# Performance work log

Measured on AMD Instinct MI355X. Metric: run time of the kernel, lower is better.

The kernel has to match this reference:

```python
import jax, jax.numpy as jnp
import numpy as np
from jax import lax

LATENT = 100
B, D, H, W = 32768, 120, 4, 2
BN_EPS = 1e-5


def setup_inputs() -> dict:
    key = jax.random.key(0)
    ks = jax.random.split(key, 12)
    inp = {
        "x1": jax.random.normal(ks[0], (B, 1, D, H, W), dtype=jnp.float32),
        "x2": jax.random.normal(ks[1], (B, 1), dtype=jnp.float32),
        "shifts": jax.random.randint(ks[2], (B, 2), 0, 5),
        "nonzero_mask_xm": jax.random.randint(ks[3], (B, 1, D, H, W), 0, 2).astype(jnp.bool_),
        # conv3d_1 / conv3d_2: Conv3d(1,1,kernel=(7,3,1)) -> OIDHW weights
        "w1": jax.random.normal(ks[4], (1, 1, 7, 3, 1), dtype=jnp.float32) * 0.2,
        "b1": jax.random.normal(ks[5], (1,), dtype=jnp.float32) * 0.1,
        "w2": jax.random.normal(ks[6], (1, 1, 7, 3, 1), dtype=jnp.float32) * 0.2,
        "b2": jax.random.normal(ks[7], (1,), dtype=jnp.float32) * 0.1,
        "fcm1_w": jax.random.normal(ks[8], (10, 80), dtype=jnp.float32) * 0.1,
        "fcm1_b": jnp.zeros((10,), dtype=jnp.float32),
        "fc_w": jax.random.normal(ks[9], (LATENT, 11), dtype=jnp.float32) * 0.3,
        "fc_b": jnp.zeros((LATENT,), dtype=jnp.float32),
    }
    return inp


def conv3d(x, w, b, pad):
    y = lax.conv_general_dilated(
        x, w, window_strides=(1, 1, 1),
        padding=[(p, p) for p in pad],
        dimension_numbers=("NCDHW", "OIDHW", "NCDHW"))
    return y + b.reshape(1, -1, 1, 1, 1)


def maxpool_d(x, k):
    # MaxPool3d((k,1,1)) with return_indices; indices flat over (D,H,W) like torch
    b, c, d, h, w = x.shape
    xr = x.reshape(b, c, d // k, k, h, w)
    vals = xr.max(axis=3)
    off = xr.argmax(axis=3)  # [b,c,d//k,h,w]
    d_idx = jnp.arange(d // k).reshape(1, 1, -1, 1, 1) * k + off
    h_idx = jnp.arange(h).reshape(1, 1, 1, -1, 1)
    w_idx = jnp.arange(w).reshape(1, 1, 1, 1, -1)
    idx = (d_idx * h + h_idx) * w + w_idx
    return vals, idx


def reference(x1, x2, shifts, nonzero_mask_xm, w1, b1, w2, b2, fcm1_w, fcm1_b, fc_w, fc_b):
    # eval-mode forward: augmentation ops are identity, rand_shift is None
    aug_xm = x1
    xm, pool1_indices = maxpool_d(jax.nn.relu(conv3d(aug_xm, w1, b1, (3, 1, 0))), 4)
    xm, pool2_indices = maxpool_d(jax.nn.relu(conv3d(xm, w2, b2, (3, 1, 0))), 3)
    xm = xm.reshape(xm.shape[0], -1)                       # [B, 80]
    xm = jnp.where(xm @ fcm1_w.T + fcm1_b > 0,
                   xm @ fcm1_w.T + fcm1_b,
                   jnp.expm1(xm @ fcm1_w.T + fcm1_b))       # ELU, [B, 10]
    aug_x_sd = x2
    x_sd = jax.nn.sigmoid(aug_x_sd)                        # [B, 1]
    xm = jnp.concatenate((xm, x_sd), axis=1)               # [B, 11]
    y = xm @ fc_w.T + fc_b                                 # [B, LATENT]
    # BatchNorm1d eval with fresh running stats (mean=0, var=1), affine=False
    z = y / jnp.sqrt(jnp.float32(1.0) + BN_EPS)
    return z, aug_xm, aug_x_sd, pool1_indices, pool2_indices
```

## Files before the change

### kernel.cpp

```cpp
#include <hip/hip_runtime.h>
#include <math.h>

#define B_TOT 32768
#define NPB 4

#define XS_RS 127
#define XS_WS (6 * XS_RS)
#define XS_SZ (2 * XS_WS)
#define P_RS 37
#define P_WS (6 * P_RS)
#define P_SZ 448

__device__ __forceinline__ void wave_sync() {
    __builtin_amdgcn_s_waitcnt(0xC07F);
    __builtin_amdgcn_wave_barrier();
}

__global__ __launch_bounds__(256) void encoder_kernel(
    const float* __restrict__ x1, const float* __restrict__ x2,
    const float* __restrict__ w1, const float* __restrict__ b1,
    const float* __restrict__ w2, const float* __restrict__ b2,
    const float* __restrict__ fcm1_w, const float* __restrict__ fcm1_b,
    const float* __restrict__ fc_w, const float* __restrict__ fc_b,
    float* __restrict__ out)
{
    __shared__ float s_fcm1w[10 * 81];
    __shared__ __align__(16) float xs[NPB][XS_SZ];
    __shared__ __align__(16) float p1[NPB][P_SZ];
    __shared__ float f2[NPB][80];
    __shared__ float v11[NPB][12];

    const int tid  = threadIdx.x;
    const int wave = tid >> 6, lane = tid & 63;
    const long b   = (long)blockIdx.x * NPB + wave;

    const size_t XM0 = (size_t)B_TOT * 100;
    const size_t SD0 = XM0 + (size_t)B_TOT * 960;
    const size_t P10 = SD0 + (size_t)B_TOT;
    const size_t P20 = P10 + (size_t)B_TOT * 240;

    for (int i = tid; i < 800; i += 256)
        s_fcm1w[(i / 80) * 81 + (i % 80)] = fcm1_w[i];
    __syncthreads();

    float w1r[21], w2r[21];
    #pragma unroll
    for (int k = 0; k < 21; k++) { w1r[k] = w1[k]; w2r[k] = w2[k]; }
    const float bb1 = b1[0], bb2 = b2[0];

    {
        const float4 z4 = make_float4(0.f, 0.f, 0.f, 0.f);
        float4* xz = (float4*)xs[wave];
        #pragma unroll
        for (int t = 0; t < 6; t++) { int i = lane + 64 * t; if (i < XS_SZ / 4) xz[i] = z4; }
        float4* pz = (float4*)p1[wave];
        #pragma unroll
        for (int t = 0; t < 2; t++) { int i = lane + 64 * t; if (i < P_SZ / 4) pz[i] = z4; }
    }
    wave_sync();

    {
        const float4* xin = (const float4*)(x1 + b * 960);
        float4*       xo  = (float4*)(out + XM0 + b * 960);
        #pragma unroll
        for (int t = 0; t < 4; t++) {
            int i = lane + 64 * t;
            if (i < 240) {
                float4 v = xin[i];
                xo[i] = v;
                float vv[4] = {v.x, v.y, v.z, v.w};
                #pragma unroll
                for (int c = 0; c < 4; c++) {
                    int e = i * 4 + c, d = e >> 3, h = (e >> 1) & 3, w = e & 1;
                    xs[wave][w * XS_WS + (h + 1) * XS_RS + d + 3] = vv[c];
                }
            }
        }
    }
    wave_sync();

    #pragma unroll
    for (int t = 0; t < 4; t++) {
        int p = lane + 64 * t;
        if (p < 240) {
            int dd = p >> 3, h = (p >> 1) & 3, w = p & 1;
            int d0 = dd * 4;
            const float* base = &xs[wave][w * XS_WS + h * XS_RS + d0];
            float vals[3][10];
            #pragma unroll
            for (int r = 0; r < 3; r++)
                #pragma unroll
                for (int c = 0; c < 10; c++)
                    vals[r][c] = base[r * XS_RS + c];
            float best = 0.f; int bj = 0;
            #pragma unroll
            for (int j = 0; j < 4; j++) {
                float acc = bb1;
                #pragma unroll
                for (int kd = 0; kd < 7; kd++)
                    #pragma unroll
                    for (int kh = 0; kh < 3; kh++)
                        acc = fmaf(vals[kh][j + kd], w1r[kd * 3 + kh], acc);
                acc = fmaxf(acc, 0.f);
                if (j == 0)            { best = acc; }
                else if (acc > best)   { best = acc; bj = j; }
            }
            p1[wave][w * P_WS + (h + 1) * P_RS + dd + 3] = best;
            out[P10 + b * 240 + p] = (float)(((dd * 4 + bj) * 4 + h) * 2 + w);
        }
    }
    wave_sync();

    #pragma unroll
    for (int t = 0; t < 2; t++) {
        int p = lane + 64 * t;
        if (p < 80) {
            int dd = p >> 3, h = (p >> 1) & 3, w = p & 1;
            int d0 = dd * 3;
            const float* base = &p1[wave][w * P_WS + h * P_RS + d0];
            float vals[3][9];
            #pragma unroll
            for (int r = 0; r < 3; r++)
                #pragma unroll
                for (int c = 0; c < 9; c++)
                    vals[r][c] = base[r * P_RS + c];
            float best = 0.f; int bj = 0;
            #pragma unroll
            for (int j = 0; j < 3; j++) {
                float acc = bb2;
                #pragma unroll
                for (int kd = 0; kd < 7; kd++)
                    #pragma unroll
                    for (int kh = 0; kh < 3; kh++)
                        acc = fmaf(vals[kh][j + kd], w2r[kd * 3 + kh], acc);
                acc = fmaxf(acc, 0.f);
                if (j == 0)            { best = acc; }
                else if (acc > best)   { best = acc; bj = j; }
            }
            f2[wave][p] = best;
            out[P20 + b * 80 + p] = (float)(((dd * 3 + bj) * 4 + h) * 2 + w);
        }
    }
    wave_sync();

    float fw0[11], fw1[11], fb0, fb1 = 0.f;
    #pragma unroll
    for (int k = 0; k < 11; k++) { fw0[k] = fc_w[lane * 11 + k]; fw1[k] = 0.f; }
    fb0 = fc_b[lane];
    if (lane < 36) {
        #pragma unroll
        for (int k = 0; k < 11; k++) fw1[k] = fc_w[(64 + lane) * 11 + k];
        fb1 = fc_b[64 + lane];
    }

    if (lane < 40) {
        int o = lane >> 2, q = lane & 3;
        float acc = 0.f;
        #pragma unroll
        for (int k = 0; k < 20; k++) {
            int i = q * 20 + k;
            acc = fmaf(f2[wave][i], s_fcm1w[o * 81 + i], acc);
        }
        acc += __shfl_xor(acc, 1);
        acc += __shfl_xor(acc, 2);
        if (q == 0) {
            acc += fcm1_b[o];
            v11[wave][o] = (acc > 0.f) ? acc : expm1f(acc);
        }
    } else if (lane == 40) {
        float xv = x2[b];
        v11[wave][10] = 1.f / (1.f + expf(-xv));
        out[SD0 + b] = xv;
    }
    wave_sync();

    {
        const float scale = 0.9999950000374997f;
        float vv[11];
        #pragma unroll
        for (int i = 0; i < 11; i++) vv[i] = v11[wave][i];
        float a0 = fb0;
        #pragma unroll
        for (int i = 0; i < 11; i++) a0 = fmaf(vv[i], fw0[i], a0);
        out[b * 100 + lane] = a0 * scale;
        if (lane < 36) {
            float a1 = fb1;
            #pragma unroll
            for (int i = 0; i < 11; i++) a1 = fmaf(vv[i], fw1[i], a1);
            out[b * 100 + 64 + lane] = a1 * scale;
        }
    }
}

extern "C" void kernel_launch(void* const* d_in, const int* in_sizes, int n_in,
                              void* d_out, int out_size, void* d_ws, size_t ws_size,
                              hipStream_t stream) {
    const float* x1     = (const float*)d_in[0];
    const float* x2     = (const float*)d_in[1];
    const float* w1     = (const float*)d_in[4];
    const float* b1     = (const float*)d_in[5];
    const float* w2     = (const float*)d_in[6];
    const float* b2     = (const float*)d_in[7];
    const float* fcm1_w = (const float*)d_in[8];
    const float* fcm1_b = (const float*)d_in[9];
    const float* fc_w   = (const float*)d_in[10];
    const float* fc_b   = (const float*)d_in[11];
    float* out = (float*)d_out;

    dim3 grid(B_TOT / NPB), block(256);
    encoder_kernel<<<grid, block, 0, stream>>>(x1, x2, w1, b1, w2, b2,
                                               fcm1_w, fcm1_b, fc_w, fc_b, out);
}
```

Measured before the change: 349.8 us.

## Shrink LDS footprint, vectorize conv1 loads, use nontemporal stores

Reorganizes shared memory so each wave uses a single buffer: the padded input stays in LDS, pool1 results are kept in registers and then written back over the same region, and f2 and v11 live at offsets inside it. The fcm1 weight staging and the block-wide __syncthreads are dropped, and those weights are read straight from global memory as float4. Conv1 reads use float4/float2 vector LDS loads from a zero row, and all output writes become nontemporal stores, with launch bounds asking for 8 blocks. The aim is more resident waves and fewer LDS and cache-pollution costs for this memory-bound kernel, at the risk of extra register pressure and uncached global weight reads.

```diff
diff --git a/kernel.cpp b/kernel.cpp
--- a/kernel.cpp
+++ b/kernel.cpp
@@ -4,19 +4,24 @@
 #define B_TOT 32768
 #define NPB 4
 
-#define XS_RS 127
-#define XS_WS (6 * XS_RS)
-#define XS_SZ (2 * XS_WS)
+#define RS1 132
+#define W1S (4 * RS1)
+#define ZROW (8 * RS1)
+#define XS_SZ 1216
+
 #define P_RS 37
-#define P_WS (6 * P_RS)
-#define P_SZ 448
+#define F2_OFF 320
+#define V11_OFF 400
+
+typedef float vf4 __attribute__((ext_vector_type(4)));
+typedef float vf2 __attribute__((ext_vector_type(2)));
 
 __device__ __forceinline__ void wave_sync() {
     __builtin_amdgcn_s_waitcnt(0xC07F);
     __builtin_amdgcn_wave_barrier();
 }
 
-__global__ __launch_bounds__(256) void encoder_kernel(
+__global__ __launch_bounds__(256, 8) void encoder_kernel(
     const float* __restrict__ x1, const float* __restrict__ x2,
     const float* __restrict__ w1, const float* __restrict__ b1,
     const float* __restrict__ w2, const float* __restrict__ b2,
@@ -24,75 +29,72 @@
     const float* __restrict__ fc_w, const float* __restrict__ fc_b,
     float* __restrict__ out)
 {
-    __shared__ float s_fcm1w[10 * 81];
     __shared__ __align__(16) float xs[NPB][XS_SZ];
-    __shared__ __align__(16) float p1[NPB][P_SZ];
-    __shared__ float f2[NPB][80];
-    __shared__ float v11[NPB][12];
 
     const int tid  = threadIdx.x;
-    const int wave = tid >> 6, lane = tid & 63;
-    const long b   = (long)blockIdx.x * NPB + wave;
+    const int wv   = tid >> 6, lane = tid & 63;
+    const long b   = (long)blockIdx.x * NPB + wv;
 
     const size_t XM0 = (size_t)B_TOT * 100;
     const size_t SD0 = XM0 + (size_t)B_TOT * 960;
     const size_t P10 = SD0 + (size_t)B_TOT;
     const size_t P20 = P10 + (size_t)B_TOT * 240;
 
-    for (int i = tid; i < 800; i += 256)
-        s_fcm1w[(i / 80) * 81 + (i % 80)] = fcm1_w[i];
-    __syncthreads();
-
     float w1r[21], w2r[21];
     #pragma unroll
     for (int k = 0; k < 21; k++) { w1r[k] = w1[k]; w2r[k] = w2[k]; }
     const float bb1 = b1[0], bb2 = b2[0];
 
     {
-        const float4 z4 = make_float4(0.f, 0.f, 0.f, 0.f);
-        float4* xz = (float4*)xs[wave];
-        #pragma unroll
-        for (int t = 0; t < 6; t++) { int i = lane + 64 * t; if (i < XS_SZ / 4) xz[i] = z4; }
-        float4* pz = (float4*)p1[wave];
-        #pragma unroll
-        for (int t = 0; t < 2; t++) { int i = lane + 64 * t; if (i < P_SZ / 4) pz[i] = z4; }
+        const vf4 z4 = (vf4){0.f, 0.f, 0.f, 0.f};
+        vf4* xz = (vf4*)xs[wv];
+        #pragma unroll
+        for (int t = 0; t < 5; t++) { int i = lane + 64 * t; if (i < XS_SZ / 4) xz[i] = z4; }
     }
     wave_sync();
 
     {
-        const float4* xin = (const float4*)(x1 + b * 960);
-        float4*       xo  = (float4*)(out + XM0 + b * 960);
+        const vf4* xin = (const vf4*)(x1 + b * 960);
+        vf4*       xo  = (vf4*)(out + XM0 + b * 960);
         #pragma unroll
         for (int t = 0; t < 4; t++) {
             int i = lane + 64 * t;
             if (i < 240) {
-                float4 v = xin[i];
-                xo[i] = v;
-                float vv[4] = {v.x, v.y, v.z, v.w};
-                #pragma unroll
-                for (int c = 0; c < 4; c++) {
-                    int e = i * 4 + c, d = e >> 3, h = (e >> 1) & 3, w = e & 1;
-                    xs[wave][w * XS_WS + (h + 1) * XS_RS + d + 3] = vv[c];
-                }
-            }
-        }
-    }
-    wave_sync();
-
+                vf4 v = xin[i];
+                __builtin_nontemporal_store(v, &xo[i]);
+                int bd = (i >> 1) + 3;
+                int hb = 2 * (i & 1);
+                xs[wv][ hb      * RS1       + bd] = v.x;
+                xs[wv][ hb      * RS1 + W1S + bd] = v.y;
+                xs[wv][(hb + 1) * RS1       + bd] = v.z;
+                xs[wv][(hb + 1) * RS1 + W1S + bd] = v.w;
+            }
+        }
+    }
+    wave_sync();
+
+    float pv[4];
     #pragma unroll
     for (int t = 0; t < 4; t++) {
         int p = lane + 64 * t;
+        float best = 0.f;
         if (p < 240) {
             int dd = p >> 3, h = (p >> 1) & 3, w = p & 1;
-            int d0 = dd * 4;
-            const float* base = &xs[wave][w * XS_WS + h * XS_RS + d0];
-            float vals[3][10];
-            #pragma unroll
-            for (int r = 0; r < 3; r++)
-                #pragma unroll
-                for (int c = 0; c < 10; c++)
-                    vals[r][c] = base[r * XS_RS + c];
-            float best = 0.f; int bj = 0;
+            int d0 = 4 * dd;
+            float va[3][10];
+            #pragma unroll
+            for (int kh = 0; kh < 3; kh++) {
+                int r = h + kh - 1;
+                int base = ((unsigned)r < 4u) ? (w * W1S + r * RS1 + d0) : (ZROW + d0);
+                const float* bp = &xs[wv][base];
+                vf4 q0 = *(const vf4*)bp;
+                vf4 q1 = *(const vf4*)(bp + 4);
+                vf2 q2 = *(const vf2*)(bp + 8);
+                va[kh][0]=q0.x; va[kh][1]=q0.y; va[kh][2]=q0.z; va[kh][3]=q0.w;
+                va[kh][4]=q1.x; va[kh][5]=q1.y; va[kh][6]=q1.z; va[kh][7]=q1.w;
+                va[kh][8]=q2.x; va[kh][9]=q2.y;
+            }
+            int bj = 0;
             #pragma unroll
             for (int j = 0; j < 4; j++) {
                 float acc = bb1;
@@ -100,13 +102,28 @@
                 for (int kd = 0; kd < 7; kd++)
                     #pragma unroll
                     for (int kh = 0; kh < 3; kh++)
-                        acc = fmaf(vals[kh][j + kd], w1r[kd * 3 + kh], acc);
+                        acc = fmaf(va[kh][j + kd], w1r[kd * 3 + kh], acc);
                 acc = fmaxf(acc, 0.f);
-                if (j == 0)            { best = acc; }
-                else if (acc > best)   { best = acc; bj = j; }
-            }
-            p1[wave][w * P_WS + (h + 1) * P_RS + dd + 3] = best;
-            out[P10 + b * 240 + p] = (float)(((dd * 4 + bj) * 4 + h) * 2 + w);
+                if (j == 0)          { best = acc; }
+                else if (acc > best) { best = acc; bj = j; }
+            }
+            __builtin_nontemporal_store(
+                (float)(((dd * 4 + bj) * 4 + h) * 2 + w), &out[P10 + b * 240 + p]);
+        }
+        pv[t] = best;
+    }
+    wave_sync();
+
+    if (lane < 48) {
+        int row = lane / 6, pos = lane - row * 6;
+        xs[wv][row * P_RS + (pos < 3 ? pos : pos + 30)] = 0.f;
+    }
+    #pragma unroll
+    for (int t = 0; t < 4; t++) {
+        int p = lane + 64 * t;
+        if (p < 240) {
+            int dd = p >> 3, h = (p >> 1) & 3, w = p & 1;
+            xs[wv][(4 * w + h) * P_RS + dd + 3] = pv[t];
         }
     }
     wave_sync();
@@ -116,14 +133,15 @@
         int p = lane + 64 * t;
         if (p < 80) {
             int dd = p >> 3, h = (p >> 1) & 3, w = p & 1;
-            int d0 = dd * 3;
-            const float* base = &p1[wave][w * P_WS + h * P_RS + d0];
-            float vals[3][9];
-            #pragma unroll
-            for (int r = 0; r < 3; r++)
+            int d0 = 3 * dd;
+            float va[3][9];
+            #pragma unroll
+            for (int kh = 0; kh < 3; kh++) {
+                int r = h + kh - 1;
+                int base = ((unsigned)r < 4u) ? ((4 * w + r) * P_RS + d0) : (ZROW + d0);
                 #pragma unroll
-                for (int c = 0; c < 9; c++)
-                    vals[r][c] = base[r * P_RS + c];
+                for (int c = 0; c < 9; c++) va[kh][c] = xs[wv][base + c];
+            }
             float best = 0.f; int bj = 0;
             #pragma unroll
             for (int j = 0; j < 3; j++) {
@@ -132,62 +150,64 @@
                 for (int kd = 0; kd < 7; kd++)
                     #pragma unroll
                     for (int kh = 0; kh < 3; kh++)
-                        acc = fmaf(vals[kh][j + kd], w2r[kd * 3 + kh], acc);
+                        acc = fmaf(va[kh][j + kd], w2r[kd * 3 + kh], acc);
                 acc = fmaxf(acc, 0.f);
-                if (j == 0)            { best = acc; }
-                else if (acc > best)   { best = acc; bj = j; }
-            }
-            f2[wave][p] = best;
-            out[P20 + b * 80 + p] = (float)(((dd * 3 + bj) * 4 + h) * 2 + w);
-        }
-    }
-    wave_sync();
-
-    float fw0[11], fw1[11], fb0, fb1 = 0.f;
-    #pragma unroll
-    for (int k = 0; k < 11; k++) { fw0[k] = fc_w[lane * 11 + k]; fw1[k] = 0.f; }
-    fb0 = fc_b[lane];
-    if (lane < 36) {
-        #pragma unroll
-        for (int k = 0; k < 11; k++) fw1[k] = fc_w[(64 + lane) * 11 + k];
-        fb1 = fc_b[64 + lane];
-    }
+                if (j == 0)          { best = acc; }
+                else if (acc > best) { best = acc; bj = j; }
+            }
+            xs[wv][F2_OFF + p] = best;
+            __builtin_nontemporal_store(
+                (float)(((dd * 3 + bj) * 4 + h) * 2 + w), &out[P20 + b * 80 + p]);
+        }
+    }
+    wave_sync();
 
     if (lane < 40) {
         int o = lane >> 2, q = lane & 3;
+        const vf4* fp = (const vf4*)&xs[wv][F2_OFF + q * 20];
+        const vf4* wp = (const vf4*)(fcm1_w + o * 80 + q * 20);
         float acc = 0.f;
         #pragma unroll
-        for (int k = 0; k < 20; k++) {
-            int i = q * 20 + k;
-            acc = fmaf(f2[wave][i], s_fcm1w[o * 81 + i], acc);
+        for (int k = 0; k < 5; k++) {
+            vf4 a = fp[k], c = wp[k];
+            acc = fmaf(a.x, c.x, fmaf(a.y, c.y, fmaf(a.z, c.z, fmaf(a.w, c.w, acc))));
         }
         acc += __shfl_xor(acc, 1);
         acc += __shfl_xor(acc, 2);
         if (q == 0) {
             acc += fcm1_b[o];
-            v11[wave][o] = (acc > 0.f) ? acc : expm1f(acc);
+            xs[wv][V11_OFF + o] = (acc > 0.f) ? acc : expm1f(acc);
         }
     } else if (lane == 40) {
         float xv = x2[b];
-        v11[wave][10] = 1.f / (1.f + expf(-xv));
-        out[SD0 + b] = xv;
+        xs[wv][V11_OFF + 10] = 1.f / (1.f + expf(-xv));
+        __builtin_nontemporal_store(xv, &out[SD0 + b]);
     }
     wave_sync();
 
     {
+        float fw0[11], fw1[11], fb0, fb1 = 0.f;
+        #pragma unroll
+        for (int k = 0; k < 11; k++) { fw0[k] = fc_w[lane * 11 + k]; fw1[k] = 0.f; }
+        fb0 = fc_b[lane];
+        if (lane < 36) {
+            #pragma unroll
+            for (int k = 0; k < 11; k++) fw1[k] = fc_w[(64 + lane) * 11 + k];
+            fb1 = fc_b[64 + lane];
+        }
         const float scale = 0.9999950000374997f;
         float vv[11];
         #pragma unroll
-        for (int i = 0; i < 11; i++) vv[i] = v11[wave][i];
+        for (int i = 0; i < 11; i++) vv[i] = xs[wv][V11_OFF + i];
         float a0 = fb0;
         #pragma unroll
         for (int i = 0; i < 11; i++) a0 = fmaf(vv[i], fw0[i], a0);
-        out[b * 100 + lane] = a0 * scale;
+        __builtin_nontemporal_store(a0 * scale, &out[b * 100 + lane]);
         if (lane < 36) {
             float a1 = fb1;
             #pragma unroll
             for (int i = 0; i < 11; i++) a1 = fmaf(vv[i], fw1[i], a1);
-            out[b * 100 + 64 + lane] = a1 * scale;
+            __builtin_nontemporal_store(a1 * scale, &out[b * 100 + 64 + lane]);
         }
     }
 }
```

After: 340.1 us. 1.03x faster.
